# Kernel optimization log

Hardware: AMD Instinct MI355X
Metric: run time of the kernel (lower is better)

Reference implementation:

```python
import jax, jax.numpy as jnp
import numpy as np

K, D, Q, N = 32, 256, 16, 4096
LOG2PI = float(np.log(2.0 * np.pi))


def setup_inputs() -> dict:
    key = jax.random.key(0)
    k1, k2, k3, k4 = jax.random.split(key, 4)
    X = jax.random.normal(k1, (N, D), dtype=jnp.float32)
    log_pi = jnp.full((K,), -np.log(K), dtype=jnp.float32)  # uniform mixture weights
    mu = 0.1 * jax.random.normal(k2, (K, D), dtype=jnp.float32)
    Lambda = 0.1 * jax.random.normal(k3, (K, D, Q), dtype=jnp.float32)
    log_psi = np.float32(np.log(0.01)) + 0.1 * jax.random.normal(k4, (K, D), dtype=jnp.float32)
    return {"X": X, "log_pi": log_pi, "mu": mu, "Lambda": Lambda, "log_psi": log_psi}


def reference(X, log_pi, mu, Lambda, log_psi):
    """MFA e_step: per-component Gaussian log-prob with C_k = L_k L_k^T + diag(psi_k) + jitter.
    Returns (log_resp_norm [N,K], log_likelihood [N]) — same math as the torch loop, batched over K."""
    d = X.shape[1]
    psi = jnp.exp(log_psi) + 1e-6                       # [K,D]
    C = jnp.einsum('kdq,keq->kde', Lambda, Lambda)       # [K,D,D] low-rank part
    C = C + jnp.eye(d, dtype=X.dtype) * (psi + 1e-5)[:, None, :]  # add diag(psi) + 1e-5 jitter
    chol = jnp.linalg.cholesky(C)                        # [K,D,D]
    diff = X[None, :, :] - mu[:, None, :]                # [K,N,D]
    # solve chol @ y = diff^T  (batched lower-triangular solve)
    y = jax.scipy.linalg.solve_triangular(chol, diff.transpose(0, 2, 1), lower=True)  # [K,D,N]
    maha = jnp.sum(y * y, axis=1)                        # [K,N]
    logdet = 2.0 * jnp.sum(jnp.log(jnp.diagonal(chol, axis1=1, axis2=2)), axis=1)  # [K]
    log_prob = -0.5 * (maha + d * LOG2PI + logdet[:, None])  # [K,N]
    log_resps = log_prob.T + log_pi[None, :]             # [N,K]
    log_likelihood = jax.scipy.special.logsumexp(log_resps, axis=1)  # [N]
    log_resp_norm = log_resps - log_likelihood[:, None]
    return log_resp_norm, log_likelihood
```

## Files before the change

kernel.cpp:

```cpp
#include <hip/hip_runtime.h>
#include <math.h>

#define KC 32
#define DD 256
#define QQ 16
#define NPTS 4096
#define LOG2PI_F 1.8378770664093453f

typedef unsigned short ushort_t;

#define OFF_VW     0
#define OFF_MINV   16384
#define OFF_U      24576
#define OFF_LOGC   25088
#define OFF_HB     25120

__device__ __forceinline__ ushort_t f2bf(float f) {
    union { float f; unsigned int u; } c; c.f = f;
    unsigned int u = c.u;
    return (ushort_t)((u + 0x7FFFu + ((u >> 16) & 1u)) >> 16);
}

#define PSTR 260
__global__ __launch_bounds__(256) void precompute_kernel(
    const float* __restrict__ log_pi, const float* __restrict__ mu,
    const float* __restrict__ Lambda, const float* __restrict__ log_psi,
    float* __restrict__ ws)
{
    __shared__ __align__(16) float sLamT[QQ * PSTR];
    __shared__ __align__(16) float sLhatT[QQ * PSTR];
    __shared__ __align__(16) float sMu[DD];
    __shared__ float sM[QQ * 17];
    __shared__ float sL[QQ * 17];
    __shared__ float sY[QQ * 17];
    __shared__ float sCol[QQ];
    __shared__ float sPart[8];
    __shared__ float sScal[2];

    const int k = blockIdx.x;
    const int tid = threadIdx.x;
    const int lane = tid & 63;
    const int wave = tid >> 6;
    ushort_t* hb = (ushort_t*)(ws + OFF_HB);
    const int d = tid;

    float Psi  = expf(log_psi[k * DD + d]) + 1.1e-5f;
    float vinv = 1.0f / Psi;
    float mud  = mu[k * DD + d];
    float wv   = vinv * mud;
    reinterpret_cast<float2*>(ws + OFF_VW + k * 2 * DD)[d] = make_float2(vinv, wv);
    sMu[d] = mud;
    float logPsi = logf(Psi);
    float ckp = wv * mud;

    float lam[QQ];
    const float4* lrow = reinterpret_cast<const float4*>(Lambda + (size_t)(k * DD + d) * QQ);
#pragma unroll
    for (int i = 0; i < 4; ++i) {
        float4 t = lrow[i];
        lam[4 * i + 0] = t.x; lam[4 * i + 1] = t.y;
        lam[4 * i + 2] = t.z; lam[4 * i + 3] = t.w;
    }
#pragma unroll
    for (int q = 0; q < QQ; ++q) {
        float lh = lam[q] * vinv;
        sLamT[q * PSTR + d]  = lam[q];
        sLhatT[q * PSTR + d] = lh;
        hb[(k * QQ + q) * DD + d] = f2bf(lh);
    }

    float r0 = logPsi, r1 = ckp;
#pragma unroll
    for (int off = 32; off >= 1; off >>= 1) {
        r0 += __shfl_down(r0, off);
        r1 += __shfl_down(r1, off);
    }
    if ((tid & 63) == 0) { sPart[wave] = r0; sPart[4 + wave] = r1; }
    __syncthreads();
    if (tid == 0) {
        sScal[0] = sPart[0] + sPart[1] + sPart[2] + sPart[3];
        sScal[1] = sPart[4] + sPart[5] + sPart[6] + sPart[7];
    }

    {
        int q = tid >> 4, r = tid & 15;
        const float4* aq = reinterpret_cast<const float4*>(sLhatT + q * PSTR);
        const float4* br = reinterpret_cast<const float4*>(sLamT + r * PSTR);
        float acc = 0.f;
#pragma unroll
        for (int i = 0; i < DD / 4; ++i) {
            float4 a = aq[i], b = br[i];
            acc += a.x * b.x + a.y * b.y + a.z * b.z + a.w * b.w;
        }
        sM[q * 17 + r] = acc + ((q == r) ? 1.0f : 0.0f);
    }
    __syncthreads();
    if (tid < QQ) {
        const float4* aq = reinterpret_cast<const float4*>(sLhatT + tid * PSTR);
        const float4* bm = reinterpret_cast<const float4*>(sMu);
        float acc = 0.f;
#pragma unroll
        for (int i = 0; i < DD / 4; ++i) {
            float4 a = aq[i], b = bm[i];
            acc += a.x * b.x + a.y * b.y + a.z * b.z + a.w * b.w;
        }
        ws[OFF_U + k * QQ + tid] = acc;
    }

    float logdetL = 0.f;
    if (wave == 0 && lane < QQ) {
        const int r = lane;
        float m[QQ];
        float l[QQ];
#pragma unroll
        for (int c = 0; c < QQ; ++c) m[c] = sM[r * 17 + c];
#pragma unroll
        for (int j = 0; j < QQ; ++j) {
            float djj = __shfl(m[j], j);
            float rinv = 1.0f / sqrtf(djj);
            l[j] = m[j] * rinv;
            sCol[r] = l[j];
#pragma unroll
            for (int c = 0; c < QQ; ++c)
                if (c > j) m[c] -= l[j] * sCol[c];
        }
#pragma unroll
        for (int j = 0; j < QQ; ++j) sL[r * 17 + j] = l[j];
        float dl = logf(l[r]);
        dl += __shfl_xor(dl, 1); dl += __shfl_xor(dl, 2);
        dl += __shfl_xor(dl, 4); dl += __shfl_xor(dl, 8);
        logdetL = dl;
        if (r == 0) sScal[0] = sScal[0];
    }
    __syncthreads();

    if (wave == 0 && lane < QQ) {
        const int c = lane;
        float y[QQ];
#pragma unroll
        for (int j = 0; j < QQ; ++j) {
            float acc = (j == c) ? 1.0f : 0.0f;
#pragma unroll
            for (int i = 0; i < QQ; ++i)
                if (i < j) acc -= sL[j * 17 + i] * y[i];
            y[j] = acc / sL[j * 17 + j];
        }
#pragma unroll
        for (int j = 0; j < QQ; ++j) sY[j * 17 + c] = y[j];
        if (c == 0) sPart[0] = logdetL;
    }
    __syncthreads();

    {
        int q = tid >> 4, r = tid & 15;
        float acc = 0.f;
#pragma unroll
        for (int j = 0; j < QQ; ++j) acc += sY[j * 17 + q] * sY[j * 17 + r];
        ws[OFF_MINV + k * QQ * QQ + tid] = acc;
    }
    if (tid == 0) {
        float logdet = sScal[0] + 2.0f * sPart[0];
        ws[OFF_LOGC + k] = log_pi[k] - 0.5f * ((float)DD * LOG2PI_F + logdet)
                         - 0.5f * sScal[1];
    }
}

#define SXF 260
#define SXH 264
#define STS 516
#define SRS 36

using short8 = __attribute__((ext_vector_type(8))) short;
using f32x4  = __attribute__((ext_vector_type(4))) float;

__global__ __launch_bounds__(256, 2) void main_kernel(
    const float* __restrict__ X, const float* __restrict__ ws,
    float* __restrict__ out)
{
    const int tid  = threadIdx.x;
    const int lane = tid & 63;
    const int wave = tid >> 6;
    const int n0   = blockIdx.x * 16;
    const ushort_t* hB = (const ushort_t*)(ws + OFF_HB);

    __shared__ __align__(16) float    sXf[16 * SXF];
    __shared__ __align__(16) ushort_t sXh[16 * SXH];
    __shared__ __align__(16) float    sT[16 * STS];
    __shared__ float sU[512];
    __shared__ float sR[16 * SRS];
    __shared__ float sLse[16];

    {
        const float4* gx = reinterpret_cast<const float4*>(X + (size_t)n0 * DD);
#pragma unroll
        for (int i = 0; i < 4; ++i) {
            int f = tid + i * 256;
            int row = f >> 6, d4 = f & 63;
            float4 v = gx[f];
            *reinterpret_cast<float4*>(sXf + row * SXF + d4 * 4) = v;
            ushort4 h = make_ushort4(f2bf(v.x), f2bf(v.y), f2bf(v.z), f2bf(v.w));
            *reinterpret_cast<ushort4*>(sXh + row * SXH + d4 * 4) = h;
        }
        sU[tid]       = ws[OFF_U + tid];
        sU[tid + 256] = ws[OFF_U + 256 + tid];
    }
    __syncthreads();

    {
        const int arow = lane & 15;
        const int quad = lane >> 4;
        f32x4 acc[8];
#pragma unroll
        for (int t = 0; t < 8; ++t) acc[t] = (f32x4){0.f, 0.f, 0.f, 0.f};

        const ushort_t* sA = sXh + arow * SXH + quad * 8;
        const ushort_t* gB = hB + (size_t)(wave * 128 + arow) * DD + quad * 8;
#pragma unroll
        for (int ks = 0; ks < 8; ++ks) {
            short8 a = *reinterpret_cast<const short8*>(sA + ks * 32);
#pragma unroll
            for (int t = 0; t < 8; ++t) {
                short8 b = *reinterpret_cast<const short8*>(gB + t * 16 * DD + ks * 32);
                acc[t] = __builtin_amdgcn_mfma_f32_16x16x32_bf16(a, b, acc[t], 0, 0, 0);
            }
        }
#pragma unroll
        for (int t = 0; t < 8; ++t) {
            int cc = wave * 128 + t * 16 + arow;
#pragma unroll
            for (int r = 0; r < 4; ++r) {
                int rr = quad * 4 + r;
                sT[rr * STS + cc] = acc[t][r] - sU[cc];
            }
        }
    }
    __syncthreads();

    {
        const int row = tid & 15, c0 = tid >> 4;
        const float4* xr = reinterpret_cast<const float4*>(sXf + row * SXF);
#pragma unroll
        for (int ci = 0; ci < 2; ++ci) {
            const int c = c0 + ci * 16;
            const float4* vw = reinterpret_cast<const float4*>(ws + OFF_VW + c * 2 * DD);
            float qx = 0.f, sx = 0.f;
#pragma unroll 8
            for (int i = 0; i < 64; ++i) {
                float4 x = xr[i];
                float4 a = vw[2 * i];
                float4 b = vw[2 * i + 1];
                qx += a.x * x.x * x.x + a.z * x.y * x.y + b.x * x.z * x.z + b.z * x.w * x.w;
                sx += a.y * x.x + a.w * x.y + b.y * x.z + b.w * x.w;
            }
            float t[QQ];
            const float* trow = sT + row * STS + c * 16;
#pragma unroll
            for (int i = 0; i < 4; ++i) {
                float4 tv = *reinterpret_cast<const float4*>(trow + i * 4);
                t[4 * i] = tv.x; t[4 * i + 1] = tv.y; t[4 * i + 2] = tv.z; t[4 * i + 3] = tv.w;
            }
            const float4* mi = reinterpret_cast<const float4*>(ws + OFF_MINV + c * 256);
            float corr = 0.f;
#pragma unroll
            for (int q = 0; q < QQ; ++q) {
                float4 m0 = mi[q * 4], m1 = mi[q * 4 + 1], m2 = mi[q * 4 + 2], m3 = mi[q * 4 + 3];
                float inner = m0.x * t[0] + m0.y * t[1] + m0.z * t[2] + m0.w * t[3]
                            + m1.x * t[4] + m1.y * t[5] + m1.z * t[6] + m1.w * t[7]
                            + m2.x * t[8] + m2.y * t[9] + m2.z * t[10] + m2.w * t[11]
                            + m3.x * t[12] + m3.y * t[13] + m3.z * t[14] + m3.w * t[15];
                corr += t[q] * inner;
            }
            float logc2 = ws[OFF_LOGC + c];
            sR[row * SRS + c] = logc2 - 0.5f * (qx - 2.0f * sx - corr);
        }
    }
    __syncthreads();

    if (tid < 16) {
        float m = -INFINITY;
#pragma unroll
        for (int c = 0; c < KC; ++c) m = fmaxf(m, sR[tid * SRS + c]);
        float sum = 0.f;
#pragma unroll
        for (int c = 0; c < KC; ++c) sum += expf(sR[tid * SRS + c] - m);
        float lse = m + logf(sum);
        sLse[tid] = lse;
        out[(size_t)NPTS * KC + n0 + tid] = lse;
    }
    __syncthreads();
    if (tid < 128) {
        int r = tid >> 3, i = tid & 7;
        float lse = sLse[r];
        float4 v = *reinterpret_cast<const float4*>(sR + r * SRS + i * 4);
        float4 o = make_float4(v.x - lse, v.y - lse, v.z - lse, v.w - lse);
        *reinterpret_cast<float4*>(out + (size_t)(n0 + r) * KC + i * 4) = o;
    }
}

extern "C" void kernel_launch(void* const* d_in, const int* in_sizes, int n_in,
                              void* d_out, int out_size, void* d_ws, size_t ws_size,
                              hipStream_t stream)
{
    (void)in_sizes; (void)n_in; (void)out_size; (void)ws_size;
    const float* X       = (const float*)d_in[0];
    const float* log_pi  = (const float*)d_in[1];
    const float* mu      = (const float*)d_in[2];
    const float* Lambda  = (const float*)d_in[3];
    const float* log_psi = (const float*)d_in[4];
    float* out = (float*)d_out;
    float* ws  = (float*)d_ws;

    precompute_kernel<<<dim3(KC), dim3(256), 0, stream>>>(log_pi, mu, Lambda, log_psi, ws);
    main_kernel<<<dim3(NPTS / 16), dim3(256), 0, stream>>>(X, ws, out);
}
```

Baseline: 96.63 us.

## Move quadratic and linear diagonal terms onto MFMA and halve rows per block

The per-component diagonal quadratic (x^2·1/psi) and linear (x·psi^-1 mu) sums were scalar fp32 loops. They are now computed as bf16 MFMA matmuls against precomputed bf16 rows of 1/psi and w. The low-rank projections and the Minv correction matrix are stored in bf16, and each block handles 8 points with 512 threads, using 16-row MFMA tiles padded with zeros. This removes most scalar FMA work and doubles the grid, but it wastes half of each MFMA tile. It also adds bf16 rounding to large-magnitude terms such as x^2/psi with psi≈0.01, which may break accuracy tolerance.

```diff
diff --git a/kernel.cpp b/kernel.cpp
--- a/kernel.cpp
+++ b/kernel.cpp
@@ -5,21 +5,27 @@
 #define DD 256
 #define QQ 16
 #define NPTS 4096
+#define NROW 8
 #define LOG2PI_F 1.8378770664093453f
 
 typedef unsigned short ushort_t;
 
-#define OFF_VW     0
-#define OFF_MINV   16384
-#define OFF_U      24576
-#define OFF_LOGC   25088
-#define OFF_HB     25120
+#define OFF_U    0
+#define OFF_LOGC 512
+#define OFF_HB   544
 
 __device__ __forceinline__ ushort_t f2bf(float f) {
     union { float f; unsigned int u; } c; c.f = f;
     unsigned int u = c.u;
     return (ushort_t)((u + 0x7FFFu + ((u >> 16) & 1u)) >> 16);
 }
+__device__ __forceinline__ float bf2f(ushort_t h) {
+    union { unsigned int u; float f; } c; c.u = ((unsigned int)h) << 16;
+    return c.f;
+}
+
+using short8 = __attribute__((ext_vector_type(8))) short;
+using f32x4  = __attribute__((ext_vector_type(4))) float;
 
 #define PSTR 260
 __global__ __launch_bounds__(256) void precompute_kernel(
@@ -48,7 +54,8 @@
     float vinv = 1.0f / Psi;
     float mud  = mu[k * DD + d];
     float wv   = vinv * mud;
-    reinterpret_cast<float2*>(ws + OFF_VW + k * 2 * DD)[d] = make_float2(vinv, wv);
+    hb[(512 + k) * DD + d] = f2bf(vinv);
+    hb[(544 + k) * DD + d] = f2bf(wv);
     sMu[d] = mud;
     float logPsi = logf(Psi);
     float ckp = wv * mud;
@@ -107,11 +114,9 @@
         ws[OFF_U + k * QQ + tid] = acc;
     }
 
-    float logdetL = 0.f;
     if (wave == 0 && lane < QQ) {
         const int r = lane;
-        float m[QQ];
-        float l[QQ];
+        float m[QQ], l[QQ];
 #pragma unroll
         for (int c = 0; c < QQ; ++c) m[c] = sM[r * 17 + c];
 #pragma unroll
@@ -129,8 +134,7 @@
         float dl = logf(l[r]);
         dl += __shfl_xor(dl, 1); dl += __shfl_xor(dl, 2);
         dl += __shfl_xor(dl, 4); dl += __shfl_xor(dl, 8);
-        logdetL = dl;
-        if (r == 0) sScal[0] = sScal[0];
+        if (r == 0) sPart[1] = dl;
     }
     __syncthreads();
 
@@ -147,7 +151,6 @@
         }
 #pragma unroll
         for (int j = 0; j < QQ; ++j) sY[j * 17 + c] = y[j];
-        if (c == 0) sPart[0] = logdetL;
     }
     __syncthreads();
 
@@ -156,127 +159,145 @@
         float acc = 0.f;
 #pragma unroll
         for (int j = 0; j < QQ; ++j) acc += sY[j * 17 + q] * sY[j * 17 + r];
-        ws[OFF_MINV + k * QQ * QQ + tid] = acc;
+        hb[(576 + k) * DD + tid] = f2bf(acc);
     }
     if (tid == 0) {
-        float logdet = sScal[0] + 2.0f * sPart[0];
+        float logdet = sScal[0] + 2.0f * sPart[1];
         ws[OFF_LOGC + k] = log_pi[k] - 0.5f * ((float)DD * LOG2PI_F + logdet)
                          - 0.5f * sScal[1];
     }
 }
 
-#define SXF 260
 #define SXH 264
-#define STS 516
+#define TSTR 520
+#define QSTR 68
 #define SRS 36
 
-using short8 = __attribute__((ext_vector_type(8))) short;
-using f32x4  = __attribute__((ext_vector_type(4))) float;
-
-__global__ __launch_bounds__(256, 2) void main_kernel(
+__global__ __launch_bounds__(512, 2) void main_kernel(
     const float* __restrict__ X, const float* __restrict__ ws,
     float* __restrict__ out)
 {
     const int tid  = threadIdx.x;
     const int lane = tid & 63;
     const int wave = tid >> 6;
-    const int n0   = blockIdx.x * 16;
+    const int n0   = blockIdx.x * NROW;
     const ushort_t* hB = (const ushort_t*)(ws + OFF_HB);
 
-    __shared__ __align__(16) float    sXf[16 * SXF];
-    __shared__ __align__(16) ushort_t sXh[16 * SXH];
-    __shared__ __align__(16) float    sT[16 * STS];
+    __shared__ __align__(16) ushort_t xh[16 * SXH];
+    __shared__ __align__(16) ushort_t sT[NROW * TSTR];
+    __shared__ __align__(16) float    sQS[NROW * QSTR];
     __shared__ float sU[512];
-    __shared__ float sR[16 * SRS];
-    __shared__ float sLse[16];
+    __shared__ float sLogc[KC];
+    __shared__ float sR[NROW * SRS];
+    __shared__ float sLse[NROW];
 
     {
         const float4* gx = reinterpret_cast<const float4*>(X + (size_t)n0 * DD);
-#pragma unroll
-        for (int i = 0; i < 4; ++i) {
-            int f = tid + i * 256;
-            int row = f >> 6, d4 = f & 63;
-            float4 v = gx[f];
-            *reinterpret_cast<float4*>(sXf + row * SXF + d4 * 4) = v;
-            ushort4 h = make_ushort4(f2bf(v.x), f2bf(v.y), f2bf(v.z), f2bf(v.w));
-            *reinterpret_cast<ushort4*>(sXh + row * SXH + d4 * 4) = h;
-        }
-        sU[tid]       = ws[OFF_U + tid];
-        sU[tid + 256] = ws[OFF_U + 256 + tid];
+        int row = tid >> 6, d4 = tid & 63;
+        float4 v = gx[tid];
+        *reinterpret_cast<ushort4*>(&xh[row * SXH + d4 * 4]) =
+            make_ushort4(f2bf(v.x), f2bf(v.y), f2bf(v.z), f2bf(v.w));
+        int zr = 8 + (tid >> 6), zc = (tid & 63) * 4;
+        *reinterpret_cast<ushort4*>(&xh[zr * SXH + zc]) = make_ushort4(0, 0, 0, 0);
+        sU[tid] = ws[OFF_U + tid];
+        if (tid < KC) sLogc[tid] = ws[OFF_LOGC + tid];
     }
     __syncthreads();
 
     {
         const int arow = lane & 15;
         const int quad = lane >> 4;
-        f32x4 acc[8];
-#pragma unroll
-        for (int t = 0; t < 8; ++t) acc[t] = (f32x4){0.f, 0.f, 0.f, 0.f};
-
-        const ushort_t* sA = sXh + arow * SXH + quad * 8;
-        const ushort_t* gB = hB + (size_t)(wave * 128 + arow) * DD + quad * 8;
-#pragma unroll
-        for (int ks = 0; ks < 8; ++ks) {
-            short8 a = *reinterpret_cast<const short8*>(sA + ks * 32);
-#pragma unroll
-            for (int t = 0; t < 8; ++t) {
-                short8 b = *reinterpret_cast<const short8*>(gB + t * 16 * DD + ks * 32);
-                acc[t] = __builtin_amdgcn_mfma_f32_16x16x32_bf16(a, b, acc[t], 0, 0, 0);
-            }
-        }
-#pragma unroll
-        for (int t = 0; t < 8; ++t) {
-            int cc = wave * 128 + t * 16 + arow;
+        short8 a[8];
+        const ushort_t* ab = xh + arow * SXH + quad * 8;
+#pragma unroll
+        for (int ks = 0; ks < 8; ++ks) a[ks] = *reinterpret_cast<const short8*>(ab + ks * 32);
+
+#pragma unroll
+        for (int i = 0; i < 4; ++i) {
+            const int tile = wave * 4 + i;
+            const ushort_t* gB = hB + (size_t)(tile * 16 + arow) * DD + quad * 8;
+            f32x4 acc = (f32x4){0.f, 0.f, 0.f, 0.f};
+#pragma unroll
+            for (int ks = 0; ks < 8; ++ks)
+                acc = __builtin_amdgcn_mfma_f32_16x16x32_bf16(
+                    a[ks], *reinterpret_cast<const short8*>(gB + ks * 32), acc, 0, 0, 0);
+            float uu = sU[tile * 16 + arow];
 #pragma unroll
             for (int r = 0; r < 4; ++r) {
                 int rr = quad * 4 + r;
-                sT[rr * STS + cc] = acc[t][r] - sU[cc];
+                if (rr < NROW) sT[rr * TSTR + tile * 16 + arow] = f2bf(acc[r] - uu);
             }
         }
-    }
-    __syncthreads();
-
-    {
-        const int row = tid & 15, c0 = tid >> 4;
-        const float4* xr = reinterpret_cast<const float4*>(sXf + row * SXF);
-#pragma unroll
-        for (int ci = 0; ci < 2; ++ci) {
-            const int c = c0 + ci * 16;
-            const float4* vw = reinterpret_cast<const float4*>(ws + OFF_VW + c * 2 * DD);
-            float qx = 0.f, sx = 0.f;
-#pragma unroll 8
-            for (int i = 0; i < 64; ++i) {
-                float4 x = xr[i];
-                float4 a = vw[2 * i];
-                float4 b = vw[2 * i + 1];
-                qx += a.x * x.x * x.x + a.z * x.y * x.y + b.x * x.z * x.z + b.z * x.w * x.w;
-                sx += a.y * x.x + a.w * x.y + b.y * x.z + b.w * x.w;
+        if (wave < 4) {
+            short8 aa[8];
+            if (wave < 2) {
+#pragma unroll
+                for (int ks = 0; ks < 8; ++ks) {
+                    short8 sq;
+#pragma unroll
+                    for (int e = 0; e < 8; ++e) {
+                        float xf = bf2f((ushort_t)a[ks][e]);
+                        sq[e] = (short)f2bf(xf * xf);
+                    }
+                    aa[ks] = sq;
+                }
+            } else {
+#pragma unroll
+                for (int ks = 0; ks < 8; ++ks) aa[ks] = a[ks];
             }
-            float t[QQ];
-            const float* trow = sT + row * STS + c * 16;
-#pragma unroll
-            for (int i = 0; i < 4; ++i) {
-                float4 tv = *reinterpret_cast<const float4*>(trow + i * 4);
-                t[4 * i] = tv.x; t[4 * i + 1] = tv.y; t[4 * i + 2] = tv.z; t[4 * i + 3] = tv.w;
+            const ushort_t* gB = hB + (size_t)(512 + wave * 16 + arow) * DD + quad * 8;
+            f32x4 acc = (f32x4){0.f, 0.f, 0.f, 0.f};
+#pragma unroll
+            for (int ks = 0; ks < 8; ++ks)
+                acc = __builtin_amdgcn_mfma_f32_16x16x32_bf16(
+                    aa[ks], *reinterpret_cast<const short8*>(gB + ks * 32), acc, 0, 0, 0);
+            const int col = (wave & 1) * 16 + arow + ((wave >> 1) & 1) * 32;
+#pragma unroll
+            for (int r = 0; r < 4; ++r) {
+                int rr = quad * 4 + r;
+                if (rr < NROW) sQS[rr * QSTR + col] = acc[r];
             }
-            const float4* mi = reinterpret_cast<const float4*>(ws + OFF_MINV + c * 256);
-            float corr = 0.f;
-#pragma unroll
-            for (int q = 0; q < QQ; ++q) {
-                float4 m0 = mi[q * 4], m1 = mi[q * 4 + 1], m2 = mi[q * 4 + 2], m3 = mi[q * 4 + 3];
-                float inner = m0.x * t[0] + m0.y * t[1] + m0.z * t[2] + m0.w * t[3]
-                            + m1.x * t[4] + m1.y * t[5] + m1.z * t[6] + m1.w * t[7]
-                            + m2.x * t[8] + m2.y * t[9] + m2.z * t[10] + m2.w * t[11]
-                            + m3.x * t[12] + m3.y * t[13] + m3.z * t[14] + m3.w * t[15];
-                corr += t[q] * inner;
+        }
+    }
+    __syncthreads();
+
+    {
+        const int half = tid & 1;
+        const int row  = (tid >> 1) & 7;
+        const int c    = (tid >> 4) & 31;
+        float t[16];
+        {
+            const ushort_t* tp = sT + row * TSTR + c * 16;
+            short8 t0 = *reinterpret_cast<const short8*>(tp);
+            short8 t1 = *reinterpret_cast<const short8*>(tp + 8);
+#pragma unroll
+            for (int e = 0; e < 8; ++e) {
+                t[e]     = bf2f((ushort_t)t0[e]);
+                t[8 + e] = bf2f((ushort_t)t1[e]);
             }
-            float logc2 = ws[OFF_LOGC + c];
-            sR[row * SRS + c] = logc2 - 0.5f * (qx - 2.0f * sx - corr);
-        }
-    }
-    __syncthreads();
-
-    if (tid < 16) {
+        }
+        const ushort_t* mp = hB + (size_t)(576 + c) * DD + half * 128;
+        float corr = 0.f;
+#pragma unroll
+        for (int q = 0; q < 8; ++q) {
+            short8 m0 = *reinterpret_cast<const short8*>(mp + q * 16);
+            short8 m1 = *reinterpret_cast<const short8*>(mp + q * 16 + 8);
+            float inner = 0.f;
+#pragma unroll
+            for (int e = 0; e < 8; ++e)
+                inner += bf2f((ushort_t)m0[e]) * t[e] + bf2f((ushort_t)m1[e]) * t[8 + e];
+            corr += t[half * 8 + q] * inner;
+        }
+        corr += __shfl_xor(corr, 1);
+        if (half == 0) {
+            float qx = sQS[row * QSTR + c];
+            float sx = sQS[row * QSTR + 32 + c];
+            sR[row * SRS + c] = sLogc[c] - 0.5f * (qx - 2.0f * sx - corr);
+        }
+    }
+    __syncthreads();
+
+    if (tid < NROW) {
         float m = -INFINITY;
 #pragma unroll
         for (int c = 0; c < KC; ++c) m = fmaxf(m, sR[tid * SRS + c]);
@@ -288,7 +309,7 @@
         out[(size_t)NPTS * KC + n0 + tid] = lse;
     }
     __syncthreads();
-    if (tid < 128) {
+    if (tid < NROW * 8) {
         int r = tid >> 3, i = tid & 7;
         float lse = sLse[r];
         float4 v = *reinterpret_cast<const float4*>(sR + r * SRS + i * 4);
@@ -311,5 +332,5 @@
     float* ws  = (float*)d_ws;
 
     precompute_kernel<<<dim3(KC), dim3(256), 0, stream>>>(log_pi, mu, Lambda, log_psi, ws);
-    main_kernel<<<dim3(NPTS / 16), dim3(256), 0, stream>>>(X, ws, out);
-}
+    main_kernel<<<dim3(NPTS / NROW), dim3(512), 0, stream>>>(X, ws, out);
+}
```

Result: no change. 94.97 us (-1.7%).
